# Kernel optimization log

Hardware: AMD Instinct MI355X
Metric: run time of the kernel (lower is better)

The kernel has to match this reference:

```python
import jax, jax.numpy as jnp
import numpy as np

D = 256        # model_dim
E = 4          # num_experts
H = 8          # attention heads
L = 8          # layers
P = 4          # patch size
IMG = 128
B = 8
NUM_CLASSES = 10
T = (IMG // P) ** 2  # 1024 tokens


def _ln(x, g, b):
    mu = jnp.mean(x, -1, keepdims=True)
    var = jnp.mean((x - mu) ** 2, -1, keepdims=True)
    return (x - mu) * jax.lax.rsqrt(var + 1e-5) * g + b


def setup_inputs() -> dict:
    key = jax.random.key(0)
    ks = jax.random.split(key, 24)
    n = lambda k, s, sc=0.02: jax.random.normal(k, s, jnp.float32) * sc
    return {
        "x": jax.random.normal(ks[0], (B, 3, IMG, IMG), jnp.float32),
        "patch_w": n(ks[1], (D, 3, P, P), 0.1),
        "patch_b": n(ks[2], (D,), 0.01),
        "pos_emb": n(ks[3], (1, T, D), 0.02),
        "router_w": n(ks[4], (E, D), 0.05),
        "router_b": n(ks[5], (E,), 0.01),
        "ln1_g": jnp.ones((L, D), jnp.float32),
        "ln1_b": jnp.zeros((L, D), jnp.float32),
        "q_w": n(ks[6], (L, D, D), 0.05),
        "q_b": n(ks[7], (L, D), 0.01),
        "k_w": n(ks[8], (L, D, D), 0.05),
        "k_b": n(ks[9], (L, D), 0.01),
        "v_w": n(ks[10], (L, D, D), 0.05),
        "v_b": n(ks[11], (L, D), 0.01),
        "o_w": n(ks[12], (L, D, D), 0.05),
        "o_b": n(ks[13], (L, D), 0.01),
        "ln2_g": jnp.ones((L, D), jnp.float32),
        "ln2_b": jnp.zeros((L, D), jnp.float32),
        "l1_w": n(ks[14], (L, 4 * D, D), 0.05),
        "l1_b": n(ks[15], (L, 4 * D), 0.01),
        "l2_w": n(ks[16], (L, D, 4 * D), 0.05),
        "l2_b": n(ks[17], (L, D), 0.01),
        "head_w": n(ks[18], (NUM_CLASSES, D), 0.05),
        "head_b": n(ks[19], (NUM_CLASSES,), 0.01),
        "alpha": jnp.full((1,), 0.5, jnp.float32),
    }


def reference(x, patch_w, patch_b, pos_emb, router_w, router_b, ln1_g, ln1_b,
              q_w, q_b, k_w, k_b, v_w, v_b, o_w, o_b, ln2_g, ln2_b,
              l1_w, l1_b, l2_w, l2_b, head_w, head_b, alpha):
    b = x.shape[0]
    # patch embed: Conv2d(3, D, P, stride=P)
    h = jax.lax.conv_general_dilated(x, patch_w, (P, P), 'VALID',
                                     dimension_numbers=('NCHW', 'OIHW', 'NCHW'))
    h = h + patch_b[None, :, None, None]
    tok = h.reshape(b, D, -1).transpose(0, 2, 1) + pos_emb   # [B,T,D]
    t = tok.shape[1]
    n_per = t // E  # uniform capacity: floor(T * 1/E)
    raw_prob = jax.nn.softmax(tok @ router_w.T + router_b, axis=-1)  # [B,T,E]
    # greedy routing: expert e takes top n_per of remaining tokens, rows zeroed after
    prob = raw_prob
    bidx = jnp.arange(b)[:, None]
    blocks, pblocks = [], []
    for e in range(E):
        _, idx = jax.lax.top_k(prob[:, :, e], n_per)            # [B,n_per]
        blocks.append(jnp.take_along_axis(tok, idx[:, :, None], axis=1))
        pblocks.append(jnp.take_along_axis(raw_prob, idx[:, :, None], axis=1))
        sel = jnp.zeros((b, t), prob.dtype).at[bidx, idx].set(1.0)
        prob = prob * (1.0 - sel)[:, :, None]
    xs = jnp.concatenate(blocks, axis=1)    # [B,T,D] expert-sorted
    rp = jnp.concatenate(pblocks, axis=1)   # [B,T,E]

    widths = [D // 2 ** e for e in range(E)]  # [256,128,64,32]
    scale = D ** -0.5                         # note: model_dim, not head_dim
    dh = D // H
    for l in range(L):
        # ---- nested-expert MHSA ----
        xn = _ln(xs, ln1_g[l], ln1_b[l])
        qs, ks_, vs = [], [], []
        for e in range(E):
            m = widths[e]
            blk = xn[:, e * n_per:(e + 1) * n_per, :m]
            qs.append(blk @ q_w[l][:, :m].T + q_b[l])
            ks_.append(blk @ k_w[l][:, :m].T + k_b[l])
            vs.append(blk @ v_w[l][:, :m].T + v_b[l])
        q = jnp.concatenate(qs, 1).reshape(b, t, H, dh).transpose(0, 2, 1, 3)
        k = jnp.concatenate(ks_, 1).reshape(b, t, H, dh).transpose(0, 2, 1, 3)
        v = jnp.concatenate(vs, 1).reshape(b, t, H, dh).transpose(0, 2, 1, 3)
        attn = jax.nn.softmax(jnp.einsum('bhqd,bhkd->bhqk', q, k) * scale, axis=-1)
        ao = jnp.einsum('bhqk,bhkd->bhqd', attn, v).transpose(0, 2, 1, 3).reshape(b, t, D)
        outs = []
        for e in range(E):
            m = widths[e]
            sl = slice(e * n_per, (e + 1) * n_per)
            o = ao[:, sl, :m] @ o_w[l][:m, :m].T + o_b[l][:m]
            o = jnp.pad(o, ((0, 0), (0, 0), (0, D - m)))
            outs.append(o + xs[:, sl, :])
        xs = jnp.concatenate(outs, 1)
        # ---- nested-expert MLP ----
        xn = _ln(xs, ln2_g[l], ln2_b[l])
        outs = []
        for e in range(E):
            m = widths[e]
            sl = slice(e * n_per, (e + 1) * n_per)
            blk = xn[:, sl, :m]
            inner = jax.nn.gelu(blk @ l1_w[l][:, :m].T + l1_b[l], approximate=False)
            outer = inner @ l2_w[l][:m, :].T + l2_b[l][:m]
            outer = jnp.pad(outer, ((0, 0), (0, 0), (0, D - m)))
            sf = (alpha[0] * rp[:, sl, e] + 1.0)[:, :, None]
            outs.append(xs[:, sl, :] + sf * outer)
        xs = jnp.concatenate(outs, 1)
    # classification head: mean pool + linear
    return jnp.mean(xs, axis=1) @ head_w.T + head_b
```

## Files before the change

kernel.cpp:

```cpp
#include <hip/hip_runtime.h>
#include <math.h>

#define D 256
#define E 4
#define H 8
#define LYR 8
#define IMG 128
#define BB 8
#define NC 10
#define T 1024
#define NPER 256
#define DH 32
#define D4 1024

using bf16x8 = __attribute__((ext_vector_type(8))) __bf16;
using bf16x4 = __attribute__((ext_vector_type(4))) __bf16;
using f32x4  = __attribute__((ext_vector_type(4))) float;

#define MFMA16(a, b, c) __builtin_amdgcn_mfma_f32_16x16x32_bf16((a), (b), (c), 0, 0, 0)
#define EXP2F(x) __builtin_exp2f(x)

__device__ __forceinline__ void gload16(const void* g, void* l) {
    __builtin_amdgcn_global_load_lds(
        (const __attribute__((address_space(1))) void*)g,
        (__attribute__((address_space(3))) void*)l, 16, 0, 0);
}

__global__ void cast6(const float* __restrict__ s0, const float* __restrict__ s1,
                      const float* __restrict__ s2, const float* __restrict__ s3,
                      const float* __restrict__ s4, const float* __restrict__ s5,
                      __bf16* __restrict__ d0, __bf16* __restrict__ d1,
                      __bf16* __restrict__ d2, __bf16* __restrict__ d3,
                      __bf16* __restrict__ d4, __bf16* __restrict__ d5) {
    const long A4 = (long)LYR * D * D / 4;
    const long W4 = (long)LYR * D4 * D / 4;
    long i = (long)blockIdx.x * 256 + threadIdx.x;
    const float* s; __bf16* d; long off;
    if (i < 4 * A4) {
        int w = (int)(i / A4); off = i - (long)w * A4;
        s = w == 0 ? s0 : w == 1 ? s1 : w == 2 ? s2 : s3;
        d = w == 0 ? d0 : w == 1 ? d1 : w == 2 ? d2 : d3;
    } else {
        long j = i - 4 * A4;
        int w = (int)(j / W4); off = j - (long)w * W4;
        s = w ? s5 : s4; d = w ? d5 : d4;
    }
    float4 v = ((const float4*)s)[off];
    bf16x4 o;
    o[0] = (__bf16)v.x; o[1] = (__bf16)v.y; o[2] = (__bf16)v.z; o[3] = (__bf16)v.w;
    ((bf16x4*)d)[off] = o;
}

__global__ void patch_router(const float* __restrict__ x, const float* __restrict__ pw,
                             const float* __restrict__ pb, const float* __restrict__ pos,
                             const float* __restrict__ rw, const float* __restrict__ rb,
                             float* __restrict__ tok, float* __restrict__ rawp) {
    int t = blockIdx.x, b = blockIdx.y, d = threadIdx.x;
    __shared__ float sx[48];
    __shared__ float srow[D];
    __shared__ float slog[4];
    int ph = t >> 5, pwc = t & 31;
    if (d < 48) {
        int c = d >> 4, ij = d & 15, i = ij >> 2, j = ij & 3;
        sx[d] = x[(((long)b * 3 + c) * IMG + (ph * 4 + i)) * IMG + (pwc * 4 + j)];
    }
    __syncthreads();
    float acc = pb[d];
    #pragma unroll
    for (int kk = 0; kk < 48; ++kk) acc += sx[kk] * pw[d * 48 + kk];
    float val = acc + pos[(long)t * D + d];
    tok[((long)b * T + t) * D + d] = val;
    srow[d] = val;
    __syncthreads();
    int wv = d >> 6, lane = d & 63;
    float a = 0.f;
    for (int c = lane; c < D; c += 64) a += srow[c] * rw[wv * D + c];
    for (int off = 32; off; off >>= 1) a += __shfl_down(a, off);
    if (lane == 0) slog[wv] = a + rb[wv];
    __syncthreads();
    if (d == 0) {
        float l0 = slog[0], l1 = slog[1], l2 = slog[2], l3 = slog[3];
        float mx = fmaxf(fmaxf(l0, l1), fmaxf(l2, l3));
        float e0 = __expf(l0 - mx), e1 = __expf(l1 - mx), e2 = __expf(l2 - mx), e3 = __expf(l3 - mx);
        float inv = 1.0f / (e0 + e1 + e2 + e3);
        long row = (long)b * T + t;
        rawp[row * 4 + 0] = e0 * inv;
        rawp[row * 4 + 1] = e1 * inv;
        rawp[row * 4 + 2] = e2 * inv;
        rawp[row * 4 + 3] = e3 * inv;
    }
}

__global__ __launch_bounds__(1024) void route_topk(const float* __restrict__ rawp,
                                                   int* __restrict__ perm,
                                                   float* __restrict__ rpsel) {
    int b = blockIdx.x, tid = threadIdx.x;
    int lane = tid & 63, wv = tid >> 6;
    __shared__ unsigned hist[256];
    __shared__ unsigned long long ball[16];
    __shared__ int sb_bin, sb_rem;
    bool assigned = false;
    for (int e = 0; e < E; ++e) {
        float v = rawp[((long)b * T + tid) * E + e];
        unsigned key = assigned ? 0u : __float_as_uint(v);
        unsigned prefix = 0;
        int rem = NPER;
        #pragma unroll
        for (int pass = 3; pass >= 0; --pass) {
            int shift = pass * 8;
            if (tid < 256) hist[tid] = 0;
            __syncthreads();
            bool active = (pass == 3) || ((key >> (shift + 8)) == prefix);
            if (active) atomicAdd(&hist[(key >> shift) & 255], 1u);
            __syncthreads();
            if (tid < 64) {
                unsigned c[4], psum = 0;
                #pragma unroll
                for (int u = 0; u < 4; ++u) { c[u] = hist[tid * 4 + u]; psum += c[u]; }
                unsigned suf = psum;
                #pragma unroll
                for (int off = 1; off < 64; off <<= 1) {
                    unsigned o = __shfl_down(suf, off);
                    if (tid + off < 64) suf += o;
                }
                unsigned El = suf - psum;
                if (El < (unsigned)rem && (unsigned)rem <= suf) {
                    unsigned cab = El;
                    #pragma unroll
                    for (int u = 3; u >= 0; --u) {
                        if ((unsigned)rem > cab && (unsigned)rem <= cab + c[u]) {
                            sb_bin = tid * 4 + u;
                            sb_rem = (int)((unsigned)rem - cab);
                        }
                        cab += c[u];
                    }
                }
            }
            __syncthreads();
            prefix = (prefix << 8) | (unsigned)sb_bin;
            rem = sb_rem;
        }
        unsigned t = prefix;
        bool is_tie = (!assigned) && (key == t);
        unsigned long long mbt = __ballot(is_tie);
        if (lane == 0) ball[wv] = mbt;
        __syncthreads();
        int tierank = 0;
        for (int w2 = 0; w2 < wv; ++w2) tierank += __popcll(ball[w2]);
        tierank += __popcll(mbt & ((1ULL << lane) - 1));
        bool sel = (!assigned) && ((key > t) || (is_tie && tierank < rem));
        __syncthreads();
        unsigned long long mbs = __ballot(sel);
        if (lane == 0) ball[wv] = mbs;
        __syncthreads();
        int rank = 0;
        for (int w2 = 0; w2 < wv; ++w2) rank += __popcll(ball[w2]);
        rank += __popcll(mbs & ((1ULL << lane) - 1));
        if (sel) {
            perm[(long)b * T + e * NPER + rank] = tid;
            rpsel[(long)b * T + e * NPER + rank] = v;
            assigned = true;
        }
        __syncthreads();
    }
}

__global__ void gather_tokens(const float* __restrict__ tok, const int* __restrict__ perm,
                              float* __restrict__ xs) {
    int slot = blockIdx.x, b = blockIdx.y, d = threadIdx.x;
    int src = perm[(long)b * T + slot];
    xs[((long)b * T + slot) * D + d] = tok[((long)b * T + src) * D + d];
}

__device__ __forceinline__ void ln_rows32(const float* __restrict__ src,
                                          const float* __restrict__ g,
                                          const float* __restrict__ bta,
                                          __bf16 (*slds)[264], int tid) {
    int sub = tid & 15, rowh = tid >> 4;
    int col0 = sub * 16;
    float gv[16], bv[16];
    #pragma unroll
    for (int u = 0; u < 4; ++u) {
        float4 gg = *(const float4*)&g[col0 + 4 * u];
        float4 bb = *(const float4*)&bta[col0 + 4 * u];
        gv[4*u] = gg.x; gv[4*u+1] = gg.y; gv[4*u+2] = gg.z; gv[4*u+3] = gg.w;
        bv[4*u] = bb.x; bv[4*u+1] = bb.y; bv[4*u+2] = bb.z; bv[4*u+3] = bb.w;
    }
    #pragma unroll
    for (int half = 0; half < 2; ++half) {
        int r = rowh + half * 16;
        const float* rp = src + (long)r * D + col0;
        float v[16];
        #pragma unroll
        for (int u = 0; u < 4; ++u) {
            float4 vv = *(const float4*)&rp[4 * u];
            v[4*u] = vv.x; v[4*u+1] = vv.y; v[4*u+2] = vv.z; v[4*u+3] = vv.w;
        }
        float s = 0.f;
        #pragma unroll
        for (int u = 0; u < 16; ++u) s += v[u];
        #pragma unroll
        for (int mk = 1; mk < 16; mk <<= 1) s += __shfl_xor(s, mk);
        float mu = s * (1.0f / D);
        float s2 = 0.f;
        #pragma unroll
        for (int u = 0; u < 16; ++u) { v[u] -= mu; s2 += v[u] * v[u]; }
        #pragma unroll
        for (int mk = 1; mk < 16; mk <<= 1) s2 += __shfl_xor(s2, mk);
        float rstd = rsqrtf(s2 * (1.0f / D) + 1e-5f);
        bf16x8 o0, o1;
        #pragma unroll
        for (int u = 0; u < 8; ++u) o0[u] = (__bf16)(v[u] * rstd * gv[u] + bv[u]);
        #pragma unroll
        for (int u = 0; u < 8; ++u) o1[u] = (__bf16)(v[8+u] * rstd * gv[8+u] + bv[8+u]);
        *(bf16x8*)&slds[r][col0]     = o0;
        *(bf16x8*)&slds[r][col0 + 8] = o1;
    }
}

template<int RG, int K>
__device__ __forceinline__ void gemm_tile(
    const __bf16* __restrict__ A, int lda,
    const __bf16* __restrict__ W, int ldb,
    int lane, f32x4 (&acc)[RG][4])
{
    int lr = lane & 15, lk = (lane >> 4) * 8;
    const __bf16* a0 = A + (long)lr * lda + lk;
    const __bf16* b0 = W + (long)lr * ldb + lk;
    const __bf16* b1 = b0 + 16 * ldb;
    const __bf16* b2 = b0 + 32 * ldb;
    const __bf16* b3 = b0 + 48 * ldb;
    constexpr int CH = (K <= 256) ? K : 128;
    for (int kb = 0; kb < K; kb += CH) {
        #pragma unroll
        for (int ku = 0; ku < CH; ku += 32) {
            int k = kb + ku;
            bf16x8 av[RG];
            #pragma unroll
            for (int i = 0; i < RG; ++i) av[i] = *(const bf16x8*)(a0 + i * 16 * lda + k);
            bf16x8 bv0 = *(const bf16x8*)(b0 + k);
            bf16x8 bv1 = *(const bf16x8*)(b1 + k);
            bf16x8 bv2 = *(const bf16x8*)(b2 + k);
            bf16x8 bv3 = *(const bf16x8*)(b3 + k);
            #pragma unroll
            for (int i = 0; i < RG; ++i) {
                acc[i][0] = MFMA16(av[i], bv0, acc[i][0]);
                acc[i][1] = MFMA16(av[i], bv1, acc[i][1]);
                acc[i][2] = MFMA16(av[i], bv2, acc[i][2]);
                acc[i][3] = MFMA16(av[i], bv3, acc[i][3]);
            }
        }
    }
}

#define GEMM_K_DISPATCH(RG, Aexpr, lda, Wexpr, ldb, accv)                        \
    switch (m) {                                                                 \
      case 256: gemm_tile<RG, 256>(Aexpr, lda, Wexpr, ldb, lane, accv); break;   \
      case 128: gemm_tile<RG, 128>(Aexpr, lda, Wexpr, ldb, lane, accv); break;   \
      case 64:  gemm_tile<RG, 64>(Aexpr, lda, Wexpr, ldb, lane, accv); break;    \
      default:  gemm_tile<RG, 32>(Aexpr, lda, Wexpr, ldb, lane, accv); break;    \
    }

__device__ __forceinline__ void tile_map(int tau, int& e, int& rt, int& ct) {
    if (tau < 64)       { e = 0; rt = tau >> 2; ct = tau & 3; }
    else if (tau < 96)  { e = 1; int t2 = tau - 64; rt = t2 >> 1; ct = t2 & 1; }
    else if (tau < 112) { e = 2; rt = tau - 96;  ct = 0; }
    else                { e = 3; rt = tau - 112; ct = 0; }
}

__global__ __launch_bounds__(256) void qkv_ln_gemm(
    const float* __restrict__ xs,
    const __bf16* __restrict__ qwb, const __bf16* __restrict__ kwb, const __bf16* __restrict__ vwb,
    const float* __restrict__ qb, const float* __restrict__ kb, const float* __restrict__ vb,
    const float* __restrict__ g, const float* __restrict__ bta,
    __bf16* __restrict__ Qb, __bf16* __restrict__ Kb, __bf16* __restrict__ Vt)
{
    int tid = threadIdx.x, lane = tid & 63, wid = tid >> 6;
    int tile = blockIdx.x, which = blockIdx.y, b = blockIdx.z;
    int row0 = tile * 32;
    int m = D >> (row0 >> 8);
    __shared__ __bf16 slds[32][264];
    ln_rows32(xs + ((long)b * T + row0) * D, g, bta, slds, tid);
    __syncthreads();
    const __bf16* W = which == 0 ? qwb : which == 1 ? kwb : vwb;
    const float* bias = which == 0 ? qb : which == 1 ? kb : vb;
    int ncol0 = wid * 64;
    const f32x4 vz = {0.f, 0.f, 0.f, 0.f};
    f32x4 acc[2][4];
    #pragma unroll
    for (int i = 0; i < 2; ++i) { acc[i][0]=vz; acc[i][1]=vz; acc[i][2]=vz; acc[i][3]=vz; }
    GEMM_K_DISPATCH(2, &slds[0][0], 264, W + (long)ncol0 * D, D, acc)
    int lr = lane & 15, rg = (lane >> 4) * 4;
    #pragma unroll
    for (int i = 0; i < 2; ++i) {
        int row = row0 + i * 16 + rg;
        #pragma unroll
        for (int j = 0; j < 4; ++j) {
            int n = ncol0 + j * 16 + lr;
            float bvs = bias[n];
            if (which == 2) {
                bf16x4 pk;
                #pragma unroll
                for (int r = 0; r < 4; ++r) pk[r] = (__bf16)(acc[i][j][r] + bvs);
                *(bf16x4*)&Vt[((long)b * D + n) * T + row] = pk;
            } else if (which == 0) {
                #pragma unroll
                for (int r = 0; r < 4; ++r)
                    Qb[((long)b * T + row + r) * D + n] =
                        (__bf16)((acc[i][j][r] + bvs) * 0.09016844005556f);
            } else {
                #pragma unroll
                for (int r = 0; r < 4; ++r)
                    Kb[((long)b * T + row + r) * D + n] = (__bf16)(acc[i][j][r] + bvs);
            }
        }
    }
}

__global__ __launch_bounds__(128) void attn_mfma(
    const __bf16* __restrict__ Qb, const __bf16* __restrict__ Kb,
    const __bf16* __restrict__ Vt, __bf16* __restrict__ aob)
{
    int bid = blockIdx.x;
    int bh = (bid & 7) * 8 + ((bid >> 3) & 7);
    int qt = bid >> 6;
    int b = bh >> 3, h = bh & 7;
    int tid = threadIdx.x;
    int lane = tid & 63, wave = tid >> 6;
    int lr = lane & 15, g = lane >> 4;
    int q0 = qt * 64 + wave * 32;
    __shared__ __bf16 plds[2][32][72];
    __shared__ __bf16 sK[2][4 * 64 * 8];
    __shared__ __bf16 sV[2][4 * 64 * 8];
    const f32x4 vz = {0.f, 0.f, 0.f, 0.f};
    bf16x8 qf[2];
    qf[0] = *(const bf16x8*)&Qb[((long)b * T + q0 + lr) * D + h * DH + g * 8];
    qf[1] = *(const bf16x8*)&Qb[((long)b * T + q0 + 16 + lr) * D + h * DH + g * 8];
    f32x4 acc[2][2] = {{vz, vz}, {vz, vz}};
    float ls[2] = {0.f, 0.f};
    int j0 = 2 * wave, j1 = 2 * wave + 1;
    const __bf16* kseg0 = Kb + ((long)b * T + 16 * j0 + lr) * D + h * DH + g * 8;
    const __bf16* kseg1 = Kb + ((long)b * T + 16 * j1 + lr) * D + h * DH + g * 8;
    const __bf16* vseg0 = Vt + ((long)b * D + h * DH + (j0 >> 1) * 16 + lr) * T
                             + 32 * (j0 & 1) + 8 * g;
    const __bf16* vseg1 = Vt + ((long)b * D + h * DH + (j1 >> 1) * 16 + lr) * T
                             + 32 * (j1 & 1) + 8 * g;

#define STAGE(BSEL, KC)                                        \
    {                                                          \
        gload16(kseg0 + (long)(KC) * D, &sK[BSEL][j0 * 512]);  \
        gload16(kseg1 + (long)(KC) * D, &sK[BSEL][j1 * 512]);  \
        gload16(vseg0 + (KC),           &sV[BSEL][j0 * 512]);  \
        gload16(vseg1 + (KC),           &sV[BSEL][j1 * 512]);  \
    }

#define COMPUTE(BSEL)                                                                     \
    {                                                                                     \
        bf16x8 kf[4], vf[2][2];                                                           \
        _Pragma("unroll")                                                                 \
        for (int j = 0; j < 4; ++j)                                                       \
            kf[j] = *(const bf16x8*)&sK[BSEL][(j * 64 + lane) * 8];                       \
        _Pragma("unroll")                                                                 \
        for (int w2 = 0; w2 < 2; ++w2)                                                    \
            _Pragma("unroll")                                                             \
            for (int df = 0; df < 2; ++df)                                                \
                vf[w2][df] = *(const bf16x8*)&sV[BSEL][((df * 2 + w2) * 64 + lane) * 8];  \
        _Pragma("unroll")                                                                 \
        for (int qi = 0; qi < 2; ++qi) {                                                  \
            _Pragma("unroll")                                                             \
            for (int j = 0; j < 4; ++j) {                                                 \
                f32x4 s = MFMA16(kf[j], qf[qi], vz);                                      \
                float p0 = EXP2F(s[0]), p1 = EXP2F(s[1]);                                 \
                float p2 = EXP2F(s[2]), p3 = EXP2F(s[3]);                                 \
                ls[qi] += (p0 + p1) + (p2 + p3);                                          \
                bf16x4 pk;                                                                \
                pk[0] = (__bf16)p0; pk[1] = (__bf16)p1;                                   \
                pk[2] = (__bf16)p2; pk[3] = (__bf16)p3;                                   \
                *(bf16x4*)&plds[wave][qi * 16 + lr][16 * j + 4 * g] = pk;                 \
            }                                                                             \
        }                                                                                 \
        _Pragma("unroll")                                                                 \
        for (int qi = 0; qi < 2; ++qi) {                                                  \
            _Pragma("unroll")                                                             \
            for (int w2 = 0; w2 < 2; ++w2) {                                              \
                bf16x8 pa = *(const bf16x8*)&plds[wave][qi * 16 + lr][32 * w2 + 8 * g];   \
                acc[qi][0] = MFMA16(pa, vf[w2][0], acc[qi][0]);                           \
                acc[qi][1] = MFMA16(pa, vf[w2][1], acc[qi][1]);                           \
            }                                                                             \
        }                                                                                 \
    }

    STAGE(0, 0)
    __syncthreads();
    int bsel = 0;
    for (int kc = 0; kc < T; kc += 64) {
        if (kc + 64 < T) STAGE(bsel ^ 1, kc + 64)
        COMPUTE(bsel)
        __syncthreads();
        bsel ^= 1;
    }
#undef STAGE
#undef COMPUTE

    #pragma unroll
    for (int qi = 0; qi < 2; ++qi) {
        ls[qi] += __shfl_xor(ls[qi], 16);
        ls[qi] += __shfl_xor(ls[qi], 32);
        float inv = 1.0f / ls[qi];
        #pragma unroll
        for (int r = 0; r < 4; ++r) {
            float invr = __shfl(inv, 4 * g + r);
            long obase = ((long)b * T + q0 + qi * 16 + 4 * g + r) * D + h * DH;
            aob[obase + lr]      = (__bf16)(acc[qi][0][r] * invr);
            aob[obase + 16 + lr] = (__bf16)(acc[qi][1][r] * invr);
        }
    }
}

__global__ __launch_bounds__(256) void oproj_gemm(
    const __bf16* __restrict__ aob, const __bf16* __restrict__ owb,
    const float* __restrict__ ob, float* __restrict__ xs)
{
    int tid = threadIdx.x, lane = tid & 63, wid = tid >> 6;
    int gw = blockIdx.x * 4 + wid;
    int b = gw >> 7, tau = gw & 127;
    int e, rt, ct;
    tile_map(tau, e, rt, ct);
    int m = D >> e;
    int row0 = e * NPER + rt * 16;
    int ncol0 = ct * 64;
    const f32x4 vz = {0.f, 0.f, 0.f, 0.f};
    f32x4 acc[1][4] = {{vz, vz, vz, vz}};
    GEMM_K_DISPATCH(1, aob + ((long)b * T + row0) * D, D, owb + (long)ncol0 * D, D, acc)
    int lr = lane & 15, rg = (lane >> 4) * 4;
    int row = row0 + rg;
    #pragma unroll
    for (int j = 0; j < 4; ++j) {
        int n = ncol0 + j * 16 + lr;
        if (n < m) {
            float bv = ob[n];
            #pragma unroll
            for (int r = 0; r < 4; ++r)
                xs[((long)b * T + row + r) * D + n] += acc[0][j][r] + bv;
        }
    }
}

__global__ __launch_bounds__(256) void mlp1_ln_gemm(
    const float* __restrict__ xs, const __bf16* __restrict__ w1b,
    const float* __restrict__ b1, const float* __restrict__ g, const float* __restrict__ bta,
    __bf16* __restrict__ innerb)
{
    int tid = threadIdx.x, lane = tid & 63, wid = tid >> 6;
    int tile = blockIdx.x, fq = blockIdx.y, b = blockIdx.z;
    int row0 = tile * 32;
    int m = D >> (row0 >> 8);
    __shared__ __bf16 slds[32][264];
    ln_rows32(xs + ((long)b * T + row0) * D, g, bta, slds, tid);
    __syncthreads();
    int ncol0 = fq * 256 + wid * 64;
    const f32x4 vz = {0.f, 0.f, 0.f, 0.f};
    f32x4 acc[2][4];
    #pragma unroll
    for (int i = 0; i < 2; ++i) { acc[i][0]=vz; acc[i][1]=vz; acc[i][2]=vz; acc[i][3]=vz; }
    GEMM_K_DISPATCH(2, &slds[0][0], 264, w1b + (long)ncol0 * D, D, acc)
    int lr = lane & 15, rg = (lane >> 4) * 4;
    #pragma unroll
    for (int i = 0; i < 2; ++i) {
        int row = row0 + i * 16 + rg;
        #pragma unroll
        for (int j = 0; j < 4; ++j) {
            int f = ncol0 + j * 16 + lr;
            float bv = b1[f];
            #pragma unroll
            for (int r = 0; r < 4; ++r) {
                float xv = acc[i][j][r] + bv;
                float gl = 0.5f * xv * (1.0f + erff(xv * 0.70710678118654752f));
                innerb[((long)b * T + row + r) * D4 + f] = (__bf16)gl;
            }
        }
    }
}

__global__ __launch_bounds__(256) void mlp2_gemm(
    const __bf16* __restrict__ innerb, const __bf16* __restrict__ w2b,
    const float* __restrict__ b2, const float* __restrict__ rpsel,
    const float* __restrict__ alpha, float* __restrict__ xs)
{
    int tid = threadIdx.x, lane = tid & 63, wid = tid >> 6;
    int gw = blockIdx.x * 4 + wid;
    int b = gw >> 7, tau = gw & 127;
    int e, rt, ct;
    tile_map(tau, e, rt, ct);
    int m = D >> e;
    int row0 = e * NPER + rt * 16;
    int ncol0 = ct * 64;
    const f32x4 vz = {0.f, 0.f, 0.f, 0.f};
    f32x4 acc[1][4] = {{vz, vz, vz, vz}};
    gemm_tile<1, 1024>(innerb + ((long)b * T + row0) * D4, D4,
                       w2b + (long)ncol0 * D4, D4, lane, acc);
    int lr = lane & 15, rg = (lane >> 4) * 4;
    int row = row0 + rg;
    float a0 = alpha[0];
    float sf[4];
    #pragma unroll
    for (int r = 0; r < 4; ++r) sf[r] = a0 * rpsel[(long)b * T + row + r] + 1.0f;
    #pragma unroll
    for (int j = 0; j < 4; ++j) {
        int n = ncol0 + j * 16 + lr;
        if (n < m) {
            float bv = b2[n];
            #pragma unroll
            for (int r = 0; r < 4; ++r)
                xs[((long)b * T + row + r) * D + n] += sf[r] * (acc[0][j][r] + bv);
        }
    }
}

__global__ void head_partial(const float* __restrict__ xs, float* __restrict__ part) {
    int c = blockIdx.x, b = blockIdx.y, d = threadIdx.x;
    const float* p = xs + ((long)b * T + c * 128) * D + d;
    float s = 0.f;
    #pragma unroll 8
    for (int i = 0; i < 128; ++i) s += p[(long)i * D];
    part[((long)b * 8 + c) * D + d] = s;
}

__global__ void head_final(const float* __restrict__ part, const float* __restrict__ hw,
                           const float* __restrict__ hb, float* __restrict__ out) {
    int b = blockIdx.x, d = threadIdx.x;
    __shared__ float smean[D];
    float s = 0.f;
    #pragma unroll
    for (int c = 0; c < 8; ++c) s += part[((long)b * 8 + c) * D + d];
    smean[d] = s * (1.0f / T);
    __syncthreads();
    if (d < NC) {
        float acc = hb[d];
        for (int c = 0; c < D; ++c) acc += smean[c] * hw[d * D + c];
        out[b * NC + d] = acc;
    }
}

extern "C" void kernel_launch(void* const* d_in, const int* in_sizes, int n_in,
                              void* d_out, int out_size, void* d_ws, size_t ws_size,
                              hipStream_t stream) {
    const float* x      = (const float*)d_in[0];
    const float* patchw = (const float*)d_in[1];
    const float* patchb = (const float*)d_in[2];
    const float* pos    = (const float*)d_in[3];
    const float* rw     = (const float*)d_in[4];
    const float* rb     = (const float*)d_in[5];
    const float* ln1g   = (const float*)d_in[6];
    const float* ln1b   = (const float*)d_in[7];
    const float* qw     = (const float*)d_in[8];
    const float* qbi    = (const float*)d_in[9];
    const float* kw     = (const float*)d_in[10];
    const float* kbi    = (const float*)d_in[11];
    const float* vw     = (const float*)d_in[12];
    const float* vbi    = (const float*)d_in[13];
    const float* ow     = (const float*)d_in[14];
    const float* obi    = (const float*)d_in[15];
    const float* ln2g   = (const float*)d_in[16];
    const float* ln2b   = (const float*)d_in[17];
    const float* l1w    = (const float*)d_in[18];
    const float* l1b    = (const float*)d_in[19];
    const float* l2w    = (const float*)d_in[20];
    const float* l2b    = (const float*)d_in[21];
    const float* hw     = (const float*)d_in[22];
    const float* hb     = (const float*)d_in[23];
    const float* alpha  = (const float*)d_in[24];

    char* p = (char*)d_ws;
    auto alloc = [&](size_t bytes) { void* r = (void*)p; p += (bytes + 255) & ~(size_t)255; return r; };
    const long NTD = (long)BB * T * D;

    float*  tok    = (float*)alloc(NTD * 4);
    float*  xs     = (float*)alloc(NTD * 4);
    float*  rawp   = (float*)alloc((long)BB * T * E * 4);
    float*  rpsel  = (float*)alloc((long)BB * T * 4);
    int*    perm   = (int*)alloc((long)BB * T * 4);
    float*  part   = (float*)alloc((long)BB * 8 * D * 4);
    __bf16* Qb     = (__bf16*)alloc(NTD * 2);
    __bf16* Kb     = (__bf16*)alloc(NTD * 2);
    __bf16* Vt     = (__bf16*)alloc(NTD * 2);
    __bf16* aob    = (__bf16*)alloc(NTD * 2);
    __bf16* innerb = (__bf16*)alloc((long)BB * T * D4 * 2);
    __bf16* qwb    = (__bf16*)alloc((long)LYR * D * D * 2);
    __bf16* kwb    = (__bf16*)alloc((long)LYR * D * D * 2);
    __bf16* vwb    = (__bf16*)alloc((long)LYR * D * D * 2);
    __bf16* owb    = (__bf16*)alloc((long)LYR * D * D * 2);
    __bf16* w1b    = (__bf16*)alloc((long)LYR * D4 * D * 2);
    __bf16* w2b    = (__bf16*)alloc((long)LYR * D * D4 * 2);

    cast6<<<6144, 256, 0, stream>>>(qw, kw, vw, ow, l1w, l2w, qwb, kwb, vwb, owb, w1b, w2b);

    patch_router<<<dim3(T, BB), 256, 0, stream>>>(x, patchw, patchb, pos, rw, rb, tok, rawp);
    route_topk<<<BB, 1024, 0, stream>>>(rawp, perm, rpsel);
    gather_tokens<<<dim3(T, BB), 256, 0, stream>>>(tok, perm, xs);

    for (int l = 0; l < LYR; ++l) {
        qkv_ln_gemm<<<dim3(32, 3, BB), 256, 0, stream>>>(
            xs, qwb + (long)l * D * D, kwb + (long)l * D * D, vwb + (long)l * D * D,
            qbi + l * D, kbi + l * D, vbi + l * D,
            ln1g + l * D, ln1b + l * D, Qb, Kb, Vt);
        attn_mfma<<<dim3(1024), 128, 0, stream>>>(Qb, Kb, Vt, aob);
        oproj_gemm<<<dim3(256), 256, 0, stream>>>(
            aob, owb + (long)l * D * D, obi + l * D, xs);
        mlp1_ln_gemm<<<dim3(32, 4, BB), 256, 0, stream>>>(
            xs, w1b + (long)l * D4 * D, l1b + (long)l * D4,
            ln2g + l * D, ln2b + l * D, innerb);
        mlp2_gemm<<<dim3(256), 256, 0, stream>>>(
            innerb, w2b + (long)l * D * D4, l2b + l * D, rpsel, alpha, xs);
    }

    head_partial<<<dim3(8, BB), 256, 0, stream>>>(xs, part);
    head_final<<<BB, D, 0, stream>>>(part, hw, hb, (float*)d_out);
}
```

Baseline: 965.6 us.

## Split attention over key halves and merge partials in output projection

Attention now launches twice as many blocks, each covering half of the key sequence. Each block writes unnormalized fp32 partial outputs and row sums, with the row sums now computed by an extra MFMA against a ones vector. The output-projection GEMM sums the two partials, normalizes, casts to bf16 and feeds them to the MFMA. The aim is better occupancy on the attention kernel, at the cost of extra fp32 global traffic for the partials and a heavier load path in oproj. It relies on the existing no-max-subtraction softmax, so the partials combine by plain addition.

```diff
diff --git a/kernel.cpp b/kernel.cpp
--- a/kernel.cpp
+++ b/kernel.cpp
@@ -319,16 +319,18 @@
 
 __global__ __launch_bounds__(128) void attn_mfma(
     const __bf16* __restrict__ Qb, const __bf16* __restrict__ Kb,
-    const __bf16* __restrict__ Vt, __bf16* __restrict__ aob)
+    const __bf16* __restrict__ Vt, float* __restrict__ pacc, float* __restrict__ pls)
 {
     int bid = blockIdx.x;
     int bh = (bid & 7) * 8 + ((bid >> 3) & 7);
-    int qt = bid >> 6;
+    int qt = (bid >> 6) & 15;
+    int split = bid >> 10;
     int b = bh >> 3, h = bh & 7;
     int tid = threadIdx.x;
     int lane = tid & 63, wave = tid >> 6;
     int lr = lane & 15, g = lane >> 4;
     int q0 = qt * 64 + wave * 32;
+    int kc0 = split * 512;
     __shared__ __bf16 plds[2][32][72];
     __shared__ __bf16 sK[2][4 * 64 * 8];
     __shared__ __bf16 sV[2][4 * 64 * 8];
@@ -336,8 +338,11 @@
     bf16x8 qf[2];
     qf[0] = *(const bf16x8*)&Qb[((long)b * T + q0 + lr) * D + h * DH + g * 8];
     qf[1] = *(const bf16x8*)&Qb[((long)b * T + q0 + 16 + lr) * D + h * DH + g * 8];
+    bf16x8 ones;
+    #pragma unroll
+    for (int u = 0; u < 8; ++u) ones[u] = (__bf16)1.0f;
     f32x4 acc[2][2] = {{vz, vz}, {vz, vz}};
-    float ls[2] = {0.f, 0.f};
+    f32x4 accs[2] = {vz, vz};
     int j0 = 2 * wave, j1 = 2 * wave + 1;
     const __bf16* kseg0 = Kb + ((long)b * T + 16 * j0 + lr) * D + h * DH + g * 8;
     const __bf16* kseg1 = Kb + ((long)b * T + 16 * j1 + lr) * D + h * DH + g * 8;
@@ -372,7 +377,6 @@
                 f32x4 s = MFMA16(kf[j], qf[qi], vz);                                      \
                 float p0 = EXP2F(s[0]), p1 = EXP2F(s[1]);                                 \
                 float p2 = EXP2F(s[2]), p3 = EXP2F(s[3]);                                 \
-                ls[qi] += (p0 + p1) + (p2 + p3);                                          \
                 bf16x4 pk;                                                                \
                 pk[0] = (__bf16)p0; pk[1] = (__bf16)p1;                                   \
                 pk[2] = (__bf16)p2; pk[3] = (__bf16)p3;                                   \
@@ -386,15 +390,16 @@
                 bf16x8 pa = *(const bf16x8*)&plds[wave][qi * 16 + lr][32 * w2 + 8 * g];   \
                 acc[qi][0] = MFMA16(pa, vf[w2][0], acc[qi][0]);                           \
                 acc[qi][1] = MFMA16(pa, vf[w2][1], acc[qi][1]);                           \
+                accs[qi]   = MFMA16(pa, ones,     accs[qi]);                              \
             }                                                                             \
         }                                                                                 \
     }
 
-    STAGE(0, 0)
+    STAGE(0, kc0)
     __syncthreads();
     int bsel = 0;
-    for (int kc = 0; kc < T; kc += 64) {
-        if (kc + 64 < T) STAGE(bsel ^ 1, kc + 64)
+    for (int kc = kc0; kc < kc0 + 512; kc += 64) {
+        if (kc + 64 < kc0 + 512) STAGE(bsel ^ 1, kc + 64)
         COMPUTE(bsel)
         __syncthreads();
         bsel ^= 1;
@@ -402,24 +407,64 @@
 #undef STAGE
 #undef COMPUTE
 
+    long sb = (long)(split * BB + b);
     #pragma unroll
     for (int qi = 0; qi < 2; ++qi) {
-        ls[qi] += __shfl_xor(ls[qi], 16);
-        ls[qi] += __shfl_xor(ls[qi], 32);
-        float inv = 1.0f / ls[qi];
         #pragma unroll
         for (int r = 0; r < 4; ++r) {
-            float invr = __shfl(inv, 4 * g + r);
-            long obase = ((long)b * T + q0 + qi * 16 + 4 * g + r) * D + h * DH;
-            aob[obase + lr]      = (__bf16)(acc[qi][0][r] * invr);
-            aob[obase + 16 + lr] = (__bf16)(acc[qi][1][r] * invr);
-        }
+            long q = q0 + qi * 16 + 4 * g + r;
+            long base = (sb * T + q) * D + h * DH;
+            pacc[base + lr]      = acc[qi][0][r];
+            pacc[base + 16 + lr] = acc[qi][1][r];
+            if (lr == 0) pls[(sb * H + h) * T + q] = accs[qi][r];
+        }
+    }
+}
+
+template<int K>
+__device__ __forceinline__ void oproj_tile(
+    const float* __restrict__ P0, const float* __restrict__ P1,
+    const float* __restrict__ L0, const float* __restrict__ L1,
+    const __bf16* __restrict__ W, int lane, f32x4 (&acc)[1][4])
+{
+    int lr = lane & 15, lk = (lane >> 4) * 8;
+    const float* p0 = P0 + (long)lr * D + lk;
+    const float* p1 = P1 + (long)lr * D + lk;
+    const __bf16* b0 = W + (long)lr * D + lk;
+    const __bf16* b1 = b0 + 16 * D;
+    const __bf16* b2 = b0 + 32 * D;
+    const __bf16* b3 = b0 + 48 * D;
+    #pragma unroll
+    for (int k = 0; k < K; k += 32) {
+        int h = k >> 5;
+        float inv = 1.0f / (L0[h * T + lr] + L1[h * T + lr]);
+        float4 a0 = *(const float4*)(p0 + k);
+        float4 a1 = *(const float4*)(p0 + k + 4);
+        float4 c0 = *(const float4*)(p1 + k);
+        float4 c1 = *(const float4*)(p1 + k + 4);
+        bf16x8 av;
+        av[0] = (__bf16)((a0.x + c0.x) * inv);
+        av[1] = (__bf16)((a0.y + c0.y) * inv);
+        av[2] = (__bf16)((a0.z + c0.z) * inv);
+        av[3] = (__bf16)((a0.w + c0.w) * inv);
+        av[4] = (__bf16)((a1.x + c1.x) * inv);
+        av[5] = (__bf16)((a1.y + c1.y) * inv);
+        av[6] = (__bf16)((a1.z + c1.z) * inv);
+        av[7] = (__bf16)((a1.w + c1.w) * inv);
+        bf16x8 bv0 = *(const bf16x8*)(b0 + k);
+        bf16x8 bv1 = *(const bf16x8*)(b1 + k);
+        bf16x8 bv2 = *(const bf16x8*)(b2 + k);
+        bf16x8 bv3 = *(const bf16x8*)(b3 + k);
+        acc[0][0] = MFMA16(av, bv0, acc[0][0]);
+        acc[0][1] = MFMA16(av, bv1, acc[0][1]);
+        acc[0][2] = MFMA16(av, bv2, acc[0][2]);
+        acc[0][3] = MFMA16(av, bv3, acc[0][3]);
     }
 }
 
 __global__ __launch_bounds__(256) void oproj_gemm(
-    const __bf16* __restrict__ aob, const __bf16* __restrict__ owb,
-    const float* __restrict__ ob, float* __restrict__ xs)
+    const float* __restrict__ pacc, const float* __restrict__ pls,
+    const __bf16* __restrict__ owb, const float* __restrict__ ob, float* __restrict__ xs)
 {
     int tid = threadIdx.x, lane = tid & 63, wid = tid >> 6;
     int gw = blockIdx.x * 4 + wid;
@@ -431,7 +476,17 @@
     int ncol0 = ct * 64;
     const f32x4 vz = {0.f, 0.f, 0.f, 0.f};
     f32x4 acc[1][4] = {{vz, vz, vz, vz}};
-    GEMM_K_DISPATCH(1, aob + ((long)b * T + row0) * D, D, owb + (long)ncol0 * D, D, acc)
+    const float* P0 = pacc + ((long)b * T + row0) * D;
+    const float* P1 = pacc + ((long)(BB + b) * T + row0) * D;
+    const float* L0 = pls + (long)b * H * T + row0;
+    const float* L1 = pls + (long)(BB + b) * H * T + row0;
+    const __bf16* W = owb + (long)ncol0 * D;
+    switch (m) {
+      case 256: oproj_tile<256>(P0, P1, L0, L1, W, lane, acc); break;
+      case 128: oproj_tile<128>(P0, P1, L0, L1, W, lane, acc); break;
+      case 64:  oproj_tile<64>(P0, P1, L0, L1, W, lane, acc); break;
+      default:  oproj_tile<32>(P0, P1, L0, L1, W, lane, acc); break;
+    }
     int lr = lane & 15, rg = (lane >> 4) * 4;
     int row = row0 + rg;
     #pragma unroll
@@ -581,10 +636,11 @@
     float*  rpsel  = (float*)alloc((long)BB * T * 4);
     int*    perm   = (int*)alloc((long)BB * T * 4);
     float*  part   = (float*)alloc((long)BB * 8 * D * 4);
+    float*  pacc   = (float*)alloc(2 * NTD * 4);
+    float*  pls    = (float*)alloc((long)2 * BB * H * T * 4);
     __bf16* Qb     = (__bf16*)alloc(NTD * 2);
     __bf16* Kb     = (__bf16*)alloc(NTD * 2);
     __bf16* Vt     = (__bf16*)alloc(NTD * 2);
-    __bf16* aob    = (__bf16*)alloc(NTD * 2);
     __bf16* innerb = (__bf16*)alloc((long)BB * T * D4 * 2);
     __bf16* qwb    = (__bf16*)alloc((long)LYR * D * D * 2);
     __bf16* kwb    = (__bf16*)alloc((long)LYR * D * D * 2);
@@ -604,9 +660,9 @@
             xs, qwb + (long)l * D * D, kwb + (long)l * D * D, vwb + (long)l * D * D,
             qbi + l * D, kbi + l * D, vbi + l * D,
             ln1g + l * D, ln1b + l * D, Qb, Kb, Vt);
-        attn_mfma<<<dim3(1024), 128, 0, stream>>>(Qb, Kb, Vt, aob);
+        attn_mfma<<<dim3(2048), 128, 0, stream>>>(Qb, Kb, Vt, pacc, pls);
         oproj_gemm<<<dim3(256), 256, 0, stream>>>(
-            aob, owb + (long)l * D * D, obi + l * D, xs);
+            pacc, pls, owb + (long)l * D * D, obi + l * D, xs);
         mlp1_ln_gemm<<<dim3(32, 4, BB), 256, 0, stream>>>(
             xs, w1b + (long)l * D4 * D, l1b + (long)l * D4,
             ln2g + l * D, ln2b + l * D, innerb);
```

New measurement: 989.9 us. 1.03x slower.

## Split attention over two key halves and combine partial results

Applied to the files above, without the earlier changes.

Splits each attention block's key range into two halves, doubling the grid to 2048 blocks, so more waves are in flight. Each half writes unnormalized fp32 partial outputs and row sums to a workspace. A new combine kernel adds the halves, normalizes, and writes bf16. Row sums now come from an MFMA against a ones vector, so they are summed over the bf16-rounded probabilities instead of the fp32 values. In exchange the change adds extra fp32 global traffic (about 16 MB written and read per layer) and one more kernel launch per layer.

```diff
diff --git a/kernel.cpp b/kernel.cpp
--- a/kernel.cpp
+++ b/kernel.cpp
@@ -319,16 +319,18 @@
 
 __global__ __launch_bounds__(128) void attn_mfma(
     const __bf16* __restrict__ Qb, const __bf16* __restrict__ Kb,
-    const __bf16* __restrict__ Vt, __bf16* __restrict__ aob)
+    const __bf16* __restrict__ Vt, float* __restrict__ pacc, float* __restrict__ pls)
 {
     int bid = blockIdx.x;
     int bh = (bid & 7) * 8 + ((bid >> 3) & 7);
-    int qt = bid >> 6;
+    int qt = (bid >> 6) & 15;
+    int split = bid >> 10;
     int b = bh >> 3, h = bh & 7;
     int tid = threadIdx.x;
     int lane = tid & 63, wave = tid >> 6;
     int lr = lane & 15, g = lane >> 4;
     int q0 = qt * 64 + wave * 32;
+    int kc0 = split * 512;
     __shared__ __bf16 plds[2][32][72];
     __shared__ __bf16 sK[2][4 * 64 * 8];
     __shared__ __bf16 sV[2][4 * 64 * 8];
@@ -336,8 +338,11 @@
     bf16x8 qf[2];
     qf[0] = *(const bf16x8*)&Qb[((long)b * T + q0 + lr) * D + h * DH + g * 8];
     qf[1] = *(const bf16x8*)&Qb[((long)b * T + q0 + 16 + lr) * D + h * DH + g * 8];
+    bf16x8 ones;
+    #pragma unroll
+    for (int u = 0; u < 8; ++u) ones[u] = (__bf16)1.0f;
     f32x4 acc[2][2] = {{vz, vz}, {vz, vz}};
-    float ls[2] = {0.f, 0.f};
+    f32x4 accs[2] = {vz, vz};
     int j0 = 2 * wave, j1 = 2 * wave + 1;
     const __bf16* kseg0 = Kb + ((long)b * T + 16 * j0 + lr) * D + h * DH + g * 8;
     const __bf16* kseg1 = Kb + ((long)b * T + 16 * j1 + lr) * D + h * DH + g * 8;
@@ -372,7 +377,6 @@
                 f32x4 s = MFMA16(kf[j], qf[qi], vz);                                      \
                 float p0 = EXP2F(s[0]), p1 = EXP2F(s[1]);                                 \
                 float p2 = EXP2F(s[2]), p3 = EXP2F(s[3]);                                 \
-                ls[qi] += (p0 + p1) + (p2 + p3);                                          \
                 bf16x4 pk;                                                                \
                 pk[0] = (__bf16)p0; pk[1] = (__bf16)p1;                                   \
                 pk[2] = (__bf16)p2; pk[3] = (__bf16)p3;                                   \
@@ -386,15 +390,16 @@
                 bf16x8 pa = *(const bf16x8*)&plds[wave][qi * 16 + lr][32 * w2 + 8 * g];   \
                 acc[qi][0] = MFMA16(pa, vf[w2][0], acc[qi][0]);                           \
                 acc[qi][1] = MFMA16(pa, vf[w2][1], acc[qi][1]);                           \
+                accs[qi]   = MFMA16(pa, ones,     accs[qi]);                              \
             }                                                                             \
         }                                                                                 \
     }
 
-    STAGE(0, 0)
+    STAGE(0, kc0)
     __syncthreads();
     int bsel = 0;
-    for (int kc = 0; kc < T; kc += 64) {
-        if (kc + 64 < T) STAGE(bsel ^ 1, kc + 64)
+    for (int kc = kc0; kc < kc0 + 512; kc += 64) {
+        if (kc + 64 < kc0 + 512) STAGE(bsel ^ 1, kc + 64)
         COMPUTE(bsel)
         __syncthreads();
         bsel ^= 1;
@@ -402,19 +407,46 @@
 #undef STAGE
 #undef COMPUTE
 
+    long sb = (long)(split * BB + b);
     #pragma unroll
     for (int qi = 0; qi < 2; ++qi) {
-        ls[qi] += __shfl_xor(ls[qi], 16);
-        ls[qi] += __shfl_xor(ls[qi], 32);
-        float inv = 1.0f / ls[qi];
         #pragma unroll
         for (int r = 0; r < 4; ++r) {
-            float invr = __shfl(inv, 4 * g + r);
-            long obase = ((long)b * T + q0 + qi * 16 + 4 * g + r) * D + h * DH;
-            aob[obase + lr]      = (__bf16)(acc[qi][0][r] * invr);
-            aob[obase + 16 + lr] = (__bf16)(acc[qi][1][r] * invr);
-        }
-    }
+            long q = q0 + qi * 16 + 4 * g + r;
+            long base = (sb * T + q) * D + h * DH;
+            pacc[base + lr]      = acc[qi][0][r];
+            pacc[base + 16 + lr] = acc[qi][1][r];
+            if (lr == 0) pls[(sb * H + h) * T + q] = accs[qi][r];
+        }
+    }
+}
+
+__global__ void attn_combine(const float* __restrict__ pacc, const float* __restrict__ pls,
+                             __bf16* __restrict__ aob) {
+    long i = (long)blockIdx.x * 256 + threadIdx.x;
+    int d0 = (int)(i & 31) * 8;
+    int q  = (int)((i >> 5) & 1023);
+    int b  = (int)(i >> 15);
+    int h  = d0 >> 5;
+    long base0 = ((long)b * T + q) * D + d0;
+    long base1 = ((long)(BB + b) * T + q) * D + d0;
+    float l0 = pls[((long)b * H + h) * T + q];
+    float l1 = pls[((long)(BB + b) * H + h) * T + q];
+    float inv = 1.0f / (l0 + l1);
+    float4 a0 = *(const float4*)&pacc[base0];
+    float4 a1 = *(const float4*)&pacc[base0 + 4];
+    float4 c0 = *(const float4*)&pacc[base1];
+    float4 c1 = *(const float4*)&pacc[base1 + 4];
+    bf16x8 o;
+    o[0] = (__bf16)((a0.x + c0.x) * inv);
+    o[1] = (__bf16)((a0.y + c0.y) * inv);
+    o[2] = (__bf16)((a0.z + c0.z) * inv);
+    o[3] = (__bf16)((a0.w + c0.w) * inv);
+    o[4] = (__bf16)((a1.x + c1.x) * inv);
+    o[5] = (__bf16)((a1.y + c1.y) * inv);
+    o[6] = (__bf16)((a1.z + c1.z) * inv);
+    o[7] = (__bf16)((a1.w + c1.w) * inv);
+    *(bf16x8*)&aob[base0] = o;
 }
 
 __global__ __launch_bounds__(256) void oproj_gemm(
@@ -581,6 +613,8 @@
     float*  rpsel  = (float*)alloc((long)BB * T * 4);
     int*    perm   = (int*)alloc((long)BB * T * 4);
     float*  part   = (float*)alloc((long)BB * 8 * D * 4);
+    float*  pacc   = (float*)alloc(2 * NTD * 4);
+    float*  pls    = (float*)alloc((long)2 * BB * H * T * 4);
     __bf16* Qb     = (__bf16*)alloc(NTD * 2);
     __bf16* Kb     = (__bf16*)alloc(NTD * 2);
     __bf16* Vt     = (__bf16*)alloc(NTD * 2);
@@ -604,7 +638,8 @@
             xs, qwb + (long)l * D * D, kwb + (long)l * D * D, vwb + (long)l * D * D,
             qbi + l * D, kbi + l * D, vbi + l * D,
             ln1g + l * D, ln1b + l * D, Qb, Kb, Vt);
-        attn_mfma<<<dim3(1024), 128, 0, stream>>>(Qb, Kb, Vt, aob);
+        attn_mfma<<<dim3(2048), 128, 0, stream>>>(Qb, Kb, Vt, pacc, pls);
+        attn_combine<<<dim3(1024), 256, 0, stream>>>(pacc, pls, aob);
         oproj_gemm<<<dim3(256), 256, 0, stream>>>(
             aob, owb + (long)l * D * D, obi + l * D, xs);
         mlp1_ln_gemm<<<dim3(32, 4, BB), 256, 0, stream>>>(
```

Result: slower. 996.3 us (+3.2%).
